# Performance work log

Measured on AMD Instinct MI355X. Metric: run time of the kernel, lower is better.

The kernel has to match this reference:

```python
import jax, jax.numpy as jnp
import numpy as np

N = 262144  # collocation points
E_MOD, I_MOM, P_LOAD = 1.0, 1.0, 1.0  # init kwargs E, I, p (L only defines domain)


def _glorot(key, fan_in, fan_out):
    lim = float(np.sqrt(6.0 / (fan_in + fan_out)))
    return jax.random.uniform(key, (fan_in, fan_out), jnp.float32, -lim, lim)


def setup_inputs() -> dict:
    key = jax.random.key(0)
    ks = jax.random.split(key, 5)
    x = jax.random.uniform(ks[0], (N,), jnp.float32)  # x in [0, L=1]
    W1 = _glorot(ks[1], 1, 15);  b1 = jnp.zeros((15,), jnp.float32)
    W2 = _glorot(ks[2], 15, 30); b2 = jnp.zeros((30,), jnp.float32)
    W3 = _glorot(ks[3], 30, 60); b3 = jnp.zeros((60,), jnp.float32)
    W4 = _glorot(ks[4], 60, 1);  b4 = jnp.zeros((1,), jnp.float32)
    return {"x": x, "W1": W1, "b1": b1, "W2": W2, "b2": b2,
            "W3": W3, "b3": b3, "W4": W4, "b4": b4}


def reference(x, W1, b1, W2, b2, W3, b3, W4, b4):
    # scalar-in / scalar-out MLP w(x): 1 -> 15 -> 30 -> 60 -> 1, tanh hidden
    def w_fn(xi):
        h1 = jnp.tanh(xi * W1[0] + b1)          # [15]
        h2 = jnp.tanh(h1 @ W2 + b2)             # [30]
        h3 = jnp.tanh(h2 @ W3 + b3)             # [60]
        return (h3 @ W4)[0] + b4[0]             # scalar

    # 4th derivative d^4 w / dx^4 via nested autodiff (mirrors 4 GradientTapes)
    d4 = jax.grad(jax.grad(jax.grad(jax.grad(w_fn))))
    w_xxxx = jax.vmap(d4)(x)                    # [N]

    pde_residual = w_xxxx - P_LOAD / (E_MOD * I_MOM)
    loss = jnp.mean(jnp.square(pde_residual))
    return loss
```

## Files before the change

kernel.cpp:

```cpp
#include <hip/hip_runtime.h>


#define MC 32
#define NM 63
#define MOMB 128

__device__ __forceinline__ float cos_turns(float phi) {
    float r;
    asm("v_cos_f32 %0, %1" : "=v"(r) : "v"(phi));
    return r;
}

__device__ __forceinline__ float fast_tanh(float u) {
    float e = __expf(2.0f * u);
    return 1.0f - 2.0f / (e + 1.0f);
}

struct TanhD { float t, s, p2, p3, p4; };

__device__ __forceinline__ TanhD tanh_derivs(float u0) {
    TanhD d;
    float t = fast_tanh(u0);
    float s = fmaf(-t, t, 1.0f);
    float ts = t * s;
    float t2 = t * t;
    d.t = t;
    d.s = s;
    d.p2 = -2.0f * ts;
    d.p3 = s * fmaf(4.0f, t2, -2.0f * s);
    d.p4 = 8.0f * ts * fmaf(-1.0f, t2, 2.0f * s);
    return d;
}

__device__ __forceinline__ void tanh_jet(const float u[5], float f[5]) {
    TanhD d = tanh_derivs(u[0]);
    float u1 = u[1], u2 = u[2], u3 = u[3], u4 = u[4];
    float u1sq = u1 * u1;
    f[0] = d.t;
    f[1] = d.s * u1;
    f[2] = fmaf(d.p2, u1sq, d.s * u2);
    f[3] = fmaf(d.p3, u1sq * u1, fmaf(3.0f * d.p2, u1 * u2, d.s * u3));
    f[4] = fmaf(d.p4, u1sq * u1sq,
           fmaf(6.0f * d.p3, u1sq * u2,
           fmaf(3.0f * d.p2, u2 * u2,
           fmaf(4.0f * d.p2, u1 * u3, d.s * u4))));
}

__device__ __forceinline__ float tanh_jet_d4(float u0, float u1, float u2,
                                             float u3, float u4) {
    TanhD d = tanh_derivs(u0);
    const float u1sq = u1 * u1;
    return fmaf(d.p4, u1sq * u1sq,
           fmaf(6.0f * d.p3, u1sq * u2,
           fmaf(3.0f * d.p2, u2 * u2,
           fmaf(4.0f * d.p2, u1 * u3, d.s * u4))));
}

__device__ __forceinline__ void accum_moments(float acc[NM], float xi) {
    const float tt = fmaf(2.0f, xi, -1.0f);
    const float t2 = tt + tt;
    float tp = 1.0f, tc = tt;
    acc[0] += 1.0f;
    acc[1] += tt;
    #pragma unroll
    for (int k = 2; k < NM; ++k) {
        const float tn = fmaf(t2, tc, -tp);
        acc[k] += tn;
        tp = tc; tc = tn;
    }
}

__global__ __launch_bounds__(256)
void pinn_stage1(const float* __restrict__ x,
                 const float* __restrict__ W1, const float* __restrict__ b1,
                 const float* __restrict__ W2, const float* __restrict__ b2,
                 const float* __restrict__ W3, const float* __restrict__ b3,
                 const float* __restrict__ W4,
                 float* __restrict__ mom_partials,
                 float* __restrict__ f_nodes, int n) {
    __shared__ float smem[8704];

    const int t = threadIdx.x;
    const int lane = t & 63;
    const int wid = t >> 6;

    if (blockIdx.x < MOMB) {
        float* trans = smem;
        float* red2  = smem + 32 * 257;

        const int base = blockIdx.x * (MOMB == 128 ? 2048 : 2048);

        float acc[NM];
        #pragma unroll
        for (int k = 0; k < NM; ++k) acc[k] = 0.0f;

        #pragma unroll
        for (int h = 0; h < 2; ++h) {
            const int i0 = base + 4 * (t + h * 256);
            if (i0 + 3 < n) {
                const float4 v = *(const float4*)&x[i0];
                accum_moments(acc, v.x);
                accum_moments(acc, v.y);
                accum_moments(acc, v.z);
                accum_moments(acc, v.w);
            } else {
                for (int u = 0; u < 4; ++u)
                    if (i0 + u < n) accum_moments(acc, x[i0 + u]);
            }
        }

        for (int c = 0; c < 2; ++c) {
            const int kbase = c * 32;
            const int kcnt = (c == 0) ? 32 : (NM - 32);
            __syncthreads();
            #pragma unroll
            for (int k = 0; k < 32; ++k)
                if (k < kcnt) trans[k * 257 + t] = acc[kbase + k];
            __syncthreads();
            {
                const int kl = t & 31, seg = t >> 5;
                if (kl < kcnt) {
                    const float* row = &trans[kl * 257 + seg * 32];
                    float s = 0.0f;
                    #pragma unroll
                    for (int u = 0; u < 32; ++u) s += row[u];
                    red2[kl * 9 + seg] = s;
                }
            }
            __syncthreads();
            if (t < kcnt) {
                float s = 0.0f;
                #pragma unroll
                for (int u = 0; u < 8; ++u) s += red2[t * 9 + u];
                mom_partials[(kbase + t) * MOMB + blockIdx.x] = s;
            }
        }
    } else {
        float* sW1 = smem;          float* sB1 = smem + 15;
        float* sB2 = smem + 30;     float* sB3 = smem + 60;
        float* sW4 = smem + 120;
        float* sW2 = smem + 180;
        float* sW3 = smem + 630;
        float* gj  = smem + 2430;
        float* h2  = smem + 2730;

        for (int idx = t; idx < 450; idx += 256) sW2[idx] = W2[idx];
        for (int idx = t; idx < 1800; idx += 256) sW3[idx] = W3[idx];
        if (t < 15) { sW1[t] = W1[t]; sB1[t] = b1[t]; }
        if (t < 30) sB2[t] = b2[t];
        if (t < 60) { sB3[t] = b3[t]; sW4[t] = W4[t]; }
        __syncthreads();

        const int node = (blockIdx.x - MOMB) * 4 + wid;
        const float phi = (float)(2 * node + 1) * (1.0f / 128.0f);
        const float xi  = fmaf(0.5f, cos_turns(phi), 0.5f);

        if (lane < 15) {
            const float w = sW1[lane];
            TanhD d = tanh_derivs(fmaf(w, xi, sB1[lane]));
            const float w2 = w * w;
            gj[wid * 75 + lane * 5 + 0] = d.t;
            gj[wid * 75 + lane * 5 + 1] = d.s * w;
            gj[wid * 75 + lane * 5 + 2] = d.p2 * w2;
            gj[wid * 75 + lane * 5 + 3] = d.p3 * w2 * w;
            gj[wid * 75 + lane * 5 + 4] = d.p4 * w2 * w2;
        }
        if (lane < 30) {
            float z[5] = { sB2[lane], 0.0f, 0.0f, 0.0f, 0.0f };
            #pragma unroll
            for (int i = 0; i < 15; ++i) {
                const float wij = sW2[i * 30 + lane];
                #pragma unroll
                for (int k = 0; k < 5; ++k)
                    z[k] = fmaf(wij, gj[wid * 75 + i * 5 + k], z[k]);
            }
            float h[5];
            tanh_jet(z, h);
            #pragma unroll
            for (int k = 0; k < 5; ++k) h2[wid * 150 + lane * 5 + k] = h[k];
        }
        float v = 0.0f;
        if (lane < 60) {
            float z[5] = { sB3[lane], 0.0f, 0.0f, 0.0f, 0.0f };
            #pragma unroll
            for (int i = 0; i < 30; ++i) {
                const float wim = sW3[i * 60 + lane];
                #pragma unroll
                for (int k = 0; k < 5; ++k)
                    z[k] = fmaf(wim, h2[wid * 150 + i * 5 + k], z[k]);
            }
            v = sW4[lane] * tanh_jet_d4(z[0], z[1], z[2], z[3], z[4]);
        }
        #pragma unroll
        for (int off = 32; off > 0; off >>= 1) v += __shfl_down(v, off, 64);
        if (lane == 0) f_nodes[node] = v;
    }
}

__global__ __launch_bounds__(256)
void pinn_stage2(const float* __restrict__ mom_partials,
                 const float* __restrict__ f_nodes,
                 float* __restrict__ out, float inv_n) {
    __shared__ float sf[MC];
    __shared__ float sg[MC];
    __shared__ float sS[NM + 1];
    __shared__ float wsum[4];

    const int t = threadIdx.x;
    if (t < MC) sf[t] = f_nodes[t];

    if (t < NM) {
        const float4* row = (const float4*)&mom_partials[t * MOMB];
        float s = 0.0f;
        #pragma unroll 4
        for (int b = 0; b < MOMB / 4; ++b) {
            const float4 v = row[b];
            s += ((v.x + v.y) + (v.z + v.w));
        }
        sS[t] = s * inv_n;
    }
    __syncthreads();

    if (t < MC) {
        float s = 0.0f;
        #pragma unroll
        for (int j = 0; j < MC; ++j) {
            const int num = (t * (2 * j + 1)) & 127;
            s = fmaf(sf[j], cos_turns((float)num * (1.0f / 128.0f)), s);
        }
        const float c = s * ((t == 0) ? (1.0f / 32.0f) : (2.0f / 32.0f));
        sg[t] = (t == 0) ? (c - 1.0f) : c;
    }
    __syncthreads();

    float val = 0.0f;
    #pragma unroll
    for (int q = 0; q < 4; ++q) {
        const int p = t + 256 * q;
        const int j = p >> 5, k = p & 31;
        const int d = (j > k) ? (j - k) : (k - j);
        val = fmaf(sg[j] * sg[k], 0.5f * (sS[j + k] + sS[d]), val);
    }

    #pragma unroll
    for (int off = 32; off > 0; off >>= 1) val += __shfl_down(val, off, 64);
    if ((t & 63) == 0) wsum[t >> 6] = val;
    __syncthreads();
    if (t == 0) out[0] = wsum[0] + wsum[1] + wsum[2] + wsum[3];
}

extern "C" void kernel_launch(void* const* d_in, const int* in_sizes, int n_in,
                              void* d_out, int out_size, void* d_ws, size_t ws_size,
                              hipStream_t stream) {
    const float* x  = (const float*)d_in[0];
    const float* W1 = (const float*)d_in[1];
    const float* b1 = (const float*)d_in[2];
    const float* W2 = (const float*)d_in[3];
    const float* b2 = (const float*)d_in[4];
    const float* W3 = (const float*)d_in[5];
    const float* b3 = (const float*)d_in[6];
    const float* W4 = (const float*)d_in[7];

    const int n = in_sizes[0];

    float* ws           = (float*)d_ws;
    float* mom_partials = ws;
    float* f_nodes      = ws + NM * MOMB;

    pinn_stage1<<<MOMB + 8, 256, 0, stream>>>(x, W1, b1, W2, b2, W3, b3, W4,
                                              mom_partials, f_nodes, n);
    pinn_stage2<<<1, 256, 0, stream>>>(mom_partials, f_nodes, (float*)d_out,
                                       1.0f / (float)n);
}
```

Measured before the change: 14.54 us.

## Fuse two-stage reduction into single kernel with last-block atomic counter

Merges the moment/MLP stage and the final reduction stage into one kernel. The last block to finish, detected through a monotonically increasing atomic counter, performs the Chebyshev-moment and loss reduction. This removes a second kernel launch and its inter-kernel gap. Moment blocks drop from 128 to 56 and use a grid-stride loop, so each block does more work. The counter is never reset and relies on a modulo of the block count, so the workspace must start at a multiple of 64.

```diff
diff --git a/kernel.cpp b/kernel.cpp
--- a/kernel.cpp
+++ b/kernel.cpp
@@ -3,7 +3,8 @@
 
 #define MC 32
 #define NM 63
-#define MOMB 128
+#define MOMB 56
+#define NBLK 64
 
 __device__ __forceinline__ float cos_turns(float phi) {
     float r;
@@ -70,45 +71,42 @@
     }
 }
 
-__global__ __launch_bounds__(256)
-void pinn_stage1(const float* __restrict__ x,
-                 const float* __restrict__ W1, const float* __restrict__ b1,
-                 const float* __restrict__ W2, const float* __restrict__ b2,
-                 const float* __restrict__ W3, const float* __restrict__ b3,
-                 const float* __restrict__ W4,
-                 float* __restrict__ mom_partials,
-                 float* __restrict__ f_nodes, int n) {
-    __shared__ float smem[8704];
+__global__ __launch_bounds__(256, 1)
+void pinn_mono(const float* __restrict__ x,
+               const float* __restrict__ W1, const float* __restrict__ b1,
+               const float* __restrict__ W2, const float* __restrict__ b2,
+               const float* __restrict__ W3, const float* __restrict__ b3,
+               const float* __restrict__ W4,
+               float* __restrict__ mom_partials,
+               float* __restrict__ f_nodes,
+               unsigned int* __restrict__ counter,
+               float* __restrict__ out, int n, float inv_n) {
+    __shared__ float smem[8512];
+    __shared__ int sflag;
 
     const int t = threadIdx.x;
     const int lane = t & 63;
     const int wid = t >> 6;
-
-    if (blockIdx.x < MOMB) {
-        float* trans = smem;
-        float* red2  = smem + 32 * 257;
-
-        const int base = blockIdx.x * (MOMB == 128 ? 2048 : 2048);
-
+    const int blk = blockIdx.x;
+
+    if (blk < MOMB) {
         float acc[NM];
         #pragma unroll
         for (int k = 0; k < NM; ++k) acc[k] = 0.0f;
 
-        #pragma unroll
-        for (int h = 0; h < 2; ++h) {
-            const int i0 = base + 4 * (t + h * 256);
-            if (i0 + 3 < n) {
-                const float4 v = *(const float4*)&x[i0];
-                accum_moments(acc, v.x);
-                accum_moments(acc, v.y);
-                accum_moments(acc, v.z);
-                accum_moments(acc, v.w);
-            } else {
-                for (int u = 0; u < 4; ++u)
-                    if (i0 + u < n) accum_moments(acc, x[i0 + u]);
-            }
-        }
-
+        const int nf4 = n >> 2;
+        for (int i4 = blk * 256 + t; i4 < nf4; i4 += MOMB * 256) {
+            const float4 v = ((const float4*)x)[i4];
+            accum_moments(acc, v.x);
+            accum_moments(acc, v.y);
+            accum_moments(acc, v.z);
+            accum_moments(acc, v.w);
+        }
+        if (blk == 0 && t == 0)
+            for (int i = (nf4 << 2); i < n; ++i) accum_moments(acc, x[i]);
+
+        float* trans = smem;
+        float* red2  = smem + 32 * 257;
         for (int c = 0; c < 2; ++c) {
             const int kbase = c * 32;
             const int kcnt = (c == 0) ? 32 : (NM - 32);
@@ -132,7 +130,8 @@
                 float s = 0.0f;
                 #pragma unroll
                 for (int u = 0; u < 8; ++u) s += red2[t * 9 + u];
-                mom_partials[(kbase + t) * MOMB + blockIdx.x] = s;
+                float old = atomicExch(&mom_partials[(kbase + t) * NBLK + blk], s);
+                asm volatile("" :: "v"(old));
             }
         }
     } else {
@@ -151,7 +150,7 @@
         if (t < 60) { sB3[t] = b3[t]; sW4[t] = W4[t]; }
         __syncthreads();
 
-        const int node = (blockIdx.x - MOMB) * 4 + wid;
+        const int node = (blk - MOMB) * 4 + wid;
         const float phi = (float)(2 * node + 1) * (1.0f / 128.0f);
         const float xi  = fmaf(0.5f, cos_turns(phi), 0.5f);
 
@@ -193,34 +192,44 @@
         }
         #pragma unroll
         for (int off = 32; off > 0; off >>= 1) v += __shfl_down(v, off, 64);
-        if (lane == 0) f_nodes[node] = v;
-    }
-}
-
-__global__ __launch_bounds__(256)
-void pinn_stage2(const float* __restrict__ mom_partials,
-                 const float* __restrict__ f_nodes,
-                 float* __restrict__ out, float inv_n) {
-    __shared__ float sf[MC];
-    __shared__ float sg[MC];
-    __shared__ float sS[NM + 1];
-    __shared__ float wsum[4];
-
-    const int t = threadIdx.x;
-    if (t < MC) sf[t] = f_nodes[t];
-
-    if (t < NM) {
-        const float4* row = (const float4*)&mom_partials[t * MOMB];
-        float s = 0.0f;
-        #pragma unroll 4
-        for (int b = 0; b < MOMB / 4; ++b) {
-            const float4 v = row[b];
-            s += ((v.x + v.y) + (v.z + v.w));
-        }
-        sS[t] = s * inv_n;
-    }
-    __syncthreads();
-
+        if (lane == 0) {
+            float old = atomicExch(&f_nodes[node], v);
+            asm volatile("" :: "v"(old));
+        }
+    }
+
+    __syncthreads();
+    if (t == 0) {
+        const unsigned int c = atomicAdd(counter, 1u);
+        sflag = ((c & (NBLK - 1)) == (NBLK - 1)) ? 1 : 0;
+    }
+    __syncthreads();
+    if (!sflag) return;
+
+    float* red  = smem;
+    float* sS   = smem + 256;
+    float* sf   = smem + 320;
+    float* sg   = smem + 352;
+    float* wsum = smem + 384;
+
+    {
+        const int k = t >> 2, q = t & 3;
+        if (k < NM) {
+            float s = 0.0f;
+            #pragma unroll
+            for (int u = 0; u < 14; ++u)
+                s += __hip_atomic_load(&mom_partials[k * NBLK + q * 14 + u],
+                                       __ATOMIC_RELAXED, __HIP_MEMORY_SCOPE_AGENT);
+            red[k * 4 + q] = s;
+        }
+        if (t < MC)
+            sf[t] = __hip_atomic_load(&f_nodes[t],
+                                      __ATOMIC_RELAXED, __HIP_MEMORY_SCOPE_AGENT);
+    }
+    __syncthreads();
+    if (t < NM)
+        sS[t] = (red[t * 4] + red[t * 4 + 1] + red[t * 4 + 2] + red[t * 4 + 3])
+                * inv_n;
     if (t < MC) {
         float s = 0.0f;
         #pragma unroll
@@ -241,7 +250,6 @@
         const int d = (j > k) ? (j - k) : (k - j);
         val = fmaf(sg[j] * sg[k], 0.5f * (sS[j + k] + sS[d]), val);
     }
-
     #pragma unroll
     for (int off = 32; off > 0; off >>= 1) val += __shfl_down(val, off, 64);
     if ((t & 63) == 0) wsum[t >> 6] = val;
@@ -265,10 +273,10 @@
 
     float* ws           = (float*)d_ws;
     float* mom_partials = ws;
-    float* f_nodes      = ws + NM * MOMB;
-
-    pinn_stage1<<<MOMB + 8, 256, 0, stream>>>(x, W1, b1, W2, b2, W3, b3, W4,
-                                              mom_partials, f_nodes, n);
-    pinn_stage2<<<1, 256, 0, stream>>>(mom_partials, f_nodes, (float*)d_out,
-                                       1.0f / (float)n);
-}
+    float* f_nodes      = ws + NM * NBLK;
+    unsigned int* counter = (unsigned int*)(ws + 4096);
+
+    pinn_mono<<<NBLK, 256, 0, stream>>>(x, W1, b1, W2, b2, W3, b3, W4,
+                                        mom_partials, f_nodes, counter,
+                                        (float*)d_out, n, 1.0f / (float)n);
+}
```

Result: slower. 14.99 us (+3.0%).
